# Kernel optimization log

Hardware: AMD Instinct MI355X
Metric: run time of the kernel (lower is better)

## Reference

```python
import jax, jax.numpy as jnp
import numpy as np

B, T, E, H = 4, 2048, 1024, 16
HD = E // H  # head dim = 64

def setup_inputs() -> dict:
    key = jax.random.key(0)
    ks = jax.random.split(key, 5)
    s = 1.0 / np.sqrt(E)
    return {
        "x": jax.random.normal(ks[0], (B, T, E), dtype=jnp.float32),
        "W_attn": jax.random.uniform(ks[1], (E, 3 * E), dtype=jnp.float32, minval=-s, maxval=s),
        "b_attn": jax.random.uniform(ks[2], (3 * E,), dtype=jnp.float32, minval=-s, maxval=s),
        "W_proj": jax.random.uniform(ks[3], (E, E), dtype=jnp.float32, minval=-s, maxval=s),
        "b_proj": jax.random.uniform(ks[4], (E,), dtype=jnp.float32, minval=-s, maxval=s),
    }

def reference(x, W_attn, b_attn, W_proj, b_proj):
    b, t, e = x.shape
    qkv = x @ W_attn + b_attn                      # [B,T,3E]
    q, k, v = jnp.split(qkv, 3, axis=-1)
    # [B,T,E] -> [B,H,T,HD]
    q = q.reshape(b, t, H, HD).transpose(0, 2, 1, 3)
    k = k.reshape(b, t, H, HD).transpose(0, 2, 1, 3)
    v = v.reshape(b, t, H, HD).transpose(0, 2, 1, 3)
    att = jnp.einsum('bhqd,bhkd->bhqk', q, k) * (1.0 / np.sqrt(HD))
    causal_mask = jnp.tril(jnp.ones((t, t), dtype=bool))
    att = jnp.where(causal_mask[None, None, :, :], att, -jnp.inf)
    att = jax.nn.softmax(att, axis=-1)             # drop=0 -> dropout is identity
    y = jnp.einsum('bhqk,bhkd->bhqd', att, v)      # [B,H,T,HD]
    y = y.transpose(0, 2, 1, 3).reshape(b, t, e)
    return y @ W_proj + b_proj
```

## Files before the change

### kernel.cpp

```cpp
#include <hip/hip_runtime.h>
#include <hip/hip_bf16.h>
#include <stdint.h>


#define B_  4
#define T_  2048
#define E_  1024
#define H_  16
#define HD_ 64

typedef unsigned short u16;
typedef __bf16 bf16x8 __attribute__((ext_vector_type(8)));
typedef float f32x4 __attribute__((ext_vector_type(4)));
typedef float f32x16 __attribute__((ext_vector_type(16)));

struct alignas(8) us4 { u16 x, y, z, w; };

__device__ __forceinline__ u16 tobf(float f) {
  union { __bf16 h; u16 u; } c;
  c.h = (__bf16)f;
  return c.u;
}

__device__ __forceinline__ void gload_lds16(const void* g, void* l) {
  auto gp = reinterpret_cast<const __attribute__((address_space(1))) uint32_t*>(
      reinterpret_cast<uintptr_t>(g));
  auto lp = reinterpret_cast<__attribute__((address_space(3))) uint32_t*>(
      reinterpret_cast<uintptr_t>(l));
  __builtin_amdgcn_global_load_lds(gp, lp, 16, 0, 0);
}

__device__ __forceinline__ bf16x8 ld_frag(const u16* p) {
  return *reinterpret_cast<const bf16x8*>(p);
}

#define BARRIER() do { __builtin_amdgcn_s_barrier(); asm volatile("" ::: "memory"); } while (0)


__global__ void cvt_bf16_kernel(const float* __restrict__ in, u16* __restrict__ out, int n) {
  int i = (blockIdx.x * blockDim.x + threadIdx.x) * 4;
  if (i >= n) return;
  float4 v = *reinterpret_cast<const float4*>(in + i);
  us4 o = { tobf(v.x), tobf(v.y), tobf(v.z), tobf(v.w) };
  *reinterpret_cast<us4*>(out + i) = o;
}

__global__ void transpose_cvt_kernel(const float* __restrict__ in, u16* __restrict__ out,
                                     int K, int N) {
  __shared__ u16 tile[32][33];
  int n0 = blockIdx.x * 32, k0 = blockIdx.y * 32;
  int tx = threadIdx.x, ty = threadIdx.y;
#pragma unroll
  for (int i = 0; i < 32; i += 8)
    tile[ty + i][tx] = tobf(in[(size_t)(k0 + ty + i) * N + n0 + tx]);
  __syncthreads();
#pragma unroll
  for (int i = 0; i < 32; i += 8)
    out[(size_t)(n0 + ty + i) * K + k0 + tx] = tile[tx][ty + i];
}


template <int MODE>
__launch_bounds__(512, 2)
__global__ void gemm_kernel(const u16* __restrict__ A, const u16* __restrict__ Bt,
                            const float* __restrict__ bias,
                            u16* __restrict__ qws, u16* __restrict__ kws,
                            u16* __restrict__ vtws, float* __restrict__ out) {
  constexpr int K = 1024, NT = 16;
  __shared__ u16 Asm[3 * 8192];
  __shared__ u16 Bsm[3 * 16384];
  const int tid = threadIdx.x;
  const int wid = tid >> 6, lane = tid & 63;
  const int wm = wid >> 2, wn = wid & 3;
  const int row0 = blockIdx.x * 128, col0 = blockIdx.y * 256;

  const int sgrow = wid * 8 + (lane >> 3);
  const int sgslot = (lane & 7) ^ (lane >> 3);
  const int lrow = lane & 15, lks = lane >> 4, r7 = lrow & 7;
  const int ca0 = ((lks) ^ r7) * 8;
  const int ca1 = ((4 + lks) ^ r7) * 8;
  const int bhalf = (wn >> 1) * 8192 + (wn & 1) * 4096;

#define STG_A(sb, kt, j)                                                        \
  gload_lds16(A + (size_t)(row0 + (j) * 64 + sgrow) * K + (kt) * 64 + sgslot * 8, \
              &Asm[(sb) * 8192 + (j) * 4096 + wid * 512])
#define STG_B(sb, kt, h, j)                                                     \
  gload_lds16(Bt + (size_t)(col0 + (h) * 128 + (j) * 64 + sgrow) * K + (kt) * 64 + sgslot * 8, \
              &Bsm[(sb) * 16384 + (h) * 8192 + (j) * 4096 + wid * 512])
#define RDA(mi, cc) ld_frag(&Asm[rb * 8192 + (wm * 64 + (mi) * 16 + lrow) * 64 + (cc)])
#define RDB(ni, cc) ld_frag(&Bsm[rb * 16384 + bhalf + ((ni) * 16 + lrow) * 64 + (cc)])

  f32x4 acc[4][4] = {};

  STG_A(0, 0, 0); STG_A(0, 0, 1);
  STG_B(0, 0, 0, 0); STG_B(0, 0, 0, 1); STG_B(0, 0, 1, 0); STG_B(0, 0, 1, 1);
  STG_A(1, 1, 0); STG_A(1, 1, 1);
  STG_B(1, 1, 0, 0); STG_B(1, 1, 0, 1); STG_B(1, 1, 1, 0); STG_B(1, 1, 1, 1);
  asm volatile("s_waitcnt vmcnt(6)" ::: "memory");
  BARRIER();

  for (int t = 0; t < NT; ++t) {
    const int rb = t % 3;
    const int sb = (t + 2) % 3;
    const bool hs = (t + 2) < NT;
    const int kt = t + 2;
    bf16x8 af[4], bf[4];

    af[0] = RDA(0, ca0); af[1] = RDA(1, ca0); af[2] = RDA(2, ca0); af[3] = RDA(3, ca0);
    bf[0] = RDB(0, ca0); bf[1] = RDB(1, ca0); bf[2] = RDB(2, ca0); bf[3] = RDB(3, ca0);
    if (hs) { STG_A(sb, kt, 0); STG_A(sb, kt, 1); }
    __builtin_amdgcn_s_setprio(1);
#pragma unroll
    for (int mi = 0; mi < 4; ++mi)
#pragma unroll
      for (int ni = 0; ni < 4; ++ni)
        acc[mi][ni] = __builtin_amdgcn_mfma_f32_16x16x32_bf16(af[mi], bf[ni], acc[mi][ni], 0, 0, 0);
    __builtin_amdgcn_s_setprio(0);

    af[0] = RDA(0, ca1); af[1] = RDA(1, ca1); af[2] = RDA(2, ca1); af[3] = RDA(3, ca1);
    bf[0] = RDB(0, ca1); bf[1] = RDB(1, ca1); bf[2] = RDB(2, ca1); bf[3] = RDB(3, ca1);
    if (hs) { STG_B(sb, kt, 0, 0); STG_B(sb, kt, 0, 1); STG_B(sb, kt, 1, 0); STG_B(sb, kt, 1, 1); }
    __builtin_amdgcn_s_setprio(1);
#pragma unroll
    for (int mi = 0; mi < 4; ++mi)
#pragma unroll
      for (int ni = 0; ni < 4; ++ni)
        acc[mi][ni] = __builtin_amdgcn_mfma_f32_16x16x32_bf16(af[mi], bf[ni], acc[mi][ni], 0, 0, 0);
    __builtin_amdgcn_s_setprio(0);

    if (hs) asm volatile("s_waitcnt vmcnt(6)" ::: "memory");
    else    asm volatile("s_waitcnt vmcnt(0)" ::: "memory");
    BARRIER();
  }
#undef STG_A
#undef STG_B
#undef RDA
#undef RDB

  if constexpr (MODE == 0) {
    const int part = (col0 + wn * 64) >> 10;
    if (part < 2) {
#pragma unroll
      for (int mi = 0; mi < 4; ++mi) {
#pragma unroll
        for (int ni = 0; ni < 4; ++ni) {
          const int gr0 = row0 + wm * 64 + mi * 16 + (lane >> 4) * 4;
          const int gc = col0 + wn * 64 + ni * 16 + (lane & 15);
          const float bv = bias[gc];
          const int e = gc & 1023;
          const int h = e >> 6, d = e & 63;
#pragma unroll
          for (int r = 0; r < 4; ++r) {
            const int m = gr0 + r;
            const int b = m >> 11, tt = m & 2047;
            const float val = acc[mi][ni][r] + bv;
            const size_t bh = (size_t)(b * H_ + h);
            if (part == 0)
              qws[(bh * T_ + tt) * HD_ + d] = tobf(val * 0.1803368801f);
            else
              kws[(bh * T_ + tt) * HD_ + d] = tobf(val);
          }
        }
      }
    } else {
      u16* vt_l = &Bsm[wid * 4608];
#pragma unroll
      for (int mi = 0; mi < 4; ++mi)
#pragma unroll
        for (int ni = 0; ni < 4; ++ni) {
          const float bv = bias[col0 + wn * 64 + ni * 16 + (lane & 15)];
#pragma unroll
          for (int r = 0; r < 4; ++r)
            vt_l[(ni * 16 + (lane & 15)) * 72 + mi * 16 + (lane >> 4) * 4 + r] =
                tobf(acc[mi][ni][r] + bv);
        }
      const int e0 = col0 + wn * 64 - 2048;
      const int h = e0 >> 6;
      const int m0 = row0 + wm * 64;
      const int b = m0 >> 11, tbase = m0 & 2047;
      u16* vbase = vtws + (size_t)(b * H_ + h) * HD_ * T_;
#pragma unroll
      for (int it = 0; it < 8; ++it) {
        const int d = it * 8 + (lane >> 3);
        const uint4 vv = *reinterpret_cast<const uint4*>(&vt_l[d * 72 + (lane & 7) * 8]);
        *reinterpret_cast<uint4*>(&vbase[(size_t)d * T_ + tbase + (lane & 7) * 8]) = vv;
      }
    }
  } else {
#pragma unroll
    for (int mi = 0; mi < 4; ++mi) {
#pragma unroll
      for (int ni = 0; ni < 4; ++ni) {
        const int gr0 = row0 + wm * 64 + mi * 16 + (lane >> 4) * 4;
        const int gc = col0 + wn * 64 + ni * 16 + (lane & 15);
        const float bv = bias[gc];
#pragma unroll
        for (int r = 0; r < 4; ++r)
          out[(size_t)(gr0 + r) * E_ + gc] = acc[mi][ni][r] + bv;
      }
    }
  }
}


__launch_bounds__(256, 4)
__global__ void attn_kernel(const u16* __restrict__ q, const u16* __restrict__ k,
                            const u16* __restrict__ vt, u16* __restrict__ y) {
  __shared__ u16 kl[2][32 * 68];
  __shared__ u16 vl[2][64 * 36];
  const int tid = threadIdx.x, w = tid >> 6, lane = tid & 63;
  const int l31 = lane & 31, hi = lane >> 5;
  const bool H = hi != 0;
  const int bid = blockIdx.x;
  const int j = 15 - (bid >> 6);
  const int bh = bid & 63;
  const u16* qp = q + (size_t)bh * T_ * HD_;
  const u16* kp = k + (size_t)bh * T_ * HD_;
  const u16* vp = vt + (size_t)bh * HD_ * T_;
  const int b = bh >> 4, h = bh & 15;
  u16* yb = y + (size_t)b * T_ * E_ + h * HD_;

  const int t0 = j * 128;
  const int qbw = t0 + w * 32;
  const int nblk = (t0 + 128) >> 5;

  bf16x8 aq[4];
#pragma unroll
  for (int slot = 0; slot < 4; ++slot)
    aq[slot] = ld_frag(qp + (size_t)(qbw + l31) * HD_ + slot * 16 + hi * 8);

  f32x16 o0 = {}, o1 = {};
  float mr = -1e30f, lr = 0.f;

  const int skv = w * 8 + (lane >> 3);
  const int skc = (lane & 7) * 8;
  const int svd = w * 16 + (lane >> 2);
  const int svc = (lane & 3) * 8;

  uint4 kreg = *(const uint4*)(kp + (size_t)skv * HD_ + skc);
  uint4 vreg = *(const uint4*)(vp + (size_t)svd * T_ + svc);

  int buf = 0;
  for (int kb = 0; kb < nblk; ++kb) {
    const int kv0 = kb * 32;
    {
      u16* kd = &kl[buf][skv * 68 + skc];
      uint2 ka = {kreg.x, kreg.y}, kb2 = {kreg.z, kreg.w};
      *(uint2*)kd = ka;
      *(uint2*)(kd + 4) = kb2;
      u16* vd = &vl[buf][svd * 36 + svc];
      uint2 va = {vreg.x, vreg.y}, vb2 = {vreg.z, vreg.w};
      *(uint2*)vd = va;
      *(uint2*)(vd + 4) = vb2;
    }
    if (kb + 1 < nblk) {
      const int kvn = kv0 + 32;
      kreg = *(const uint4*)(kp + (size_t)(kvn + skv) * HD_ + skc);
      vreg = *(const uint4*)(vp + (size_t)svd * T_ + kvn + svc);
    }
    __syncthreads();

    if (kv0 <= qbw + 31) {
      f32x16 s = {};
      __builtin_amdgcn_s_setprio(1);
#pragma unroll
      for (int slot = 0; slot < 4; ++slot) {
        union { uint2 d[2]; bf16x8 v; } kf;
        const u16* kr = &kl[buf][l31 * 68 + slot * 16 + hi * 8];
        kf.d[0] = *(const uint2*)kr;
        kf.d[1] = *(const uint2*)(kr + 4);
        s = __builtin_amdgcn_mfma_f32_32x32x16_bf16(kf.v, aq[slot], s, 0, 0, 0);
      }
      __builtin_amdgcn_s_setprio(0);

      if (kv0 + 31 > qbw) {
        const int qq = qbw + l31;
#pragma unroll
        for (int r = 0; r < 16; ++r) {
          const int kv = kv0 + (r & 3) + 8 * (r >> 2) + 4 * hi;
          if (kv > qq) s[r] = -1e30f;
        }
      }

      float t[8];
#pragma unroll
      for (int r = 0; r < 8; ++r) t[r] = fmaxf(s[r], s[r + 8]);
#pragma unroll
      for (int r = 0; r < 4; ++r) t[r] = fmaxf(t[r], t[r + 4]);
      float pm = fmaxf(fmaxf(t[0], t[1]), fmaxf(t[2], t[3]));
      pm = fmaxf(pm, __shfl_xor(pm, 32));

      if (__any(pm > mr + 8.f)) {
        const float mn = fmaxf(mr, pm);
        const float al = exp2f(mr - mn);
        mr = mn;
        lr *= al;
#pragma unroll
        for (int r = 0; r < 16; ++r) {
          const float ab = __shfl(al, ((r & 3) + 8 * (r >> 2) + 4 * hi) + (lane & 32));
          o0[r] *= ab;
          o1[r] *= ab;
        }
      }

      float p[16];
      float rs = 0.f;
#pragma unroll
      for (int r = 0; r < 16; ++r) {
        p[r] = exp2f(s[r] - mr);
        rs += p[r];
      }
      rs += __shfl_xor(rs, 32);
      lr += rs;

      unsigned cw[8];
#pragma unroll
      for (int i = 0; i < 8; ++i) {
        union { __bf16 hh[2]; unsigned u; } pk;
        pk.hh[0] = (__bf16)p[2 * i];
        pk.hh[1] = (__bf16)p[2 * i + 1];
        cw[i] = pk.u;
      }
      const unsigned r0 = __shfl_xor(H ? cw[0] : cw[2], 32);
      const unsigned r1 = __shfl_xor(H ? cw[1] : cw[3], 32);
      const unsigned r2 = __shfl_xor(H ? cw[4] : cw[6], 32);
      const unsigned r3 = __shfl_xor(H ? cw[5] : cw[7], 32);
      union PU { unsigned u[4]; bf16x8 v; } pa0, pa1;
      pa0.u[0] = H ? r0 : cw[0];
      pa0.u[1] = H ? r1 : cw[1];
      pa0.u[2] = H ? cw[2] : r0;
      pa0.u[3] = H ? cw[3] : r1;
      pa1.u[0] = H ? r2 : cw[4];
      pa1.u[1] = H ? r3 : cw[5];
      pa1.u[2] = H ? cw[6] : r2;
      pa1.u[3] = H ? cw[7] : r3;

      __builtin_amdgcn_s_setprio(1);
      {
        union { uint2 d[2]; bf16x8 v; } vf;
        const u16* vr0 = &vl[buf][l31 * 36 + hi * 8];
        vf.d[0] = *(const uint2*)vr0;
        vf.d[1] = *(const uint2*)(vr0 + 4);
        o0 = __builtin_amdgcn_mfma_f32_32x32x16_bf16(pa0.v, vf.v, o0, 0, 0, 0);
        vf.d[0] = *(const uint2*)(vr0 + 16);
        vf.d[1] = *(const uint2*)(vr0 + 20);
        o0 = __builtin_amdgcn_mfma_f32_32x32x16_bf16(pa1.v, vf.v, o0, 0, 0, 0);
        const u16* vr1 = &vl[buf][(32 + l31) * 36 + hi * 8];
        vf.d[0] = *(const uint2*)vr1;
        vf.d[1] = *(const uint2*)(vr1 + 4);
        o1 = __builtin_amdgcn_mfma_f32_32x32x16_bf16(pa0.v, vf.v, o1, 0, 0, 0);
        vf.d[0] = *(const uint2*)(vr1 + 16);
        vf.d[1] = *(const uint2*)(vr1 + 20);
        o1 = __builtin_amdgcn_mfma_f32_32x32x16_bf16(pa1.v, vf.v, o1, 0, 0, 0);
      }
      __builtin_amdgcn_s_setprio(0);
    }
    buf ^= 1;
  }

  const float il = 1.f / lr;
#pragma unroll
  for (int r = 0; r < 16; ++r) {
    const int cr = (r & 3) + 8 * (r >> 2) + 4 * hi;
    const float li = __shfl(il, cr + (lane & 32));
    const size_t row = (size_t)(qbw + cr) * E_;
    yb[row + l31] = tobf(o0[r] * li);
    yb[row + 32 + l31] = tobf(o1[r] * li);
  }
}


extern "C" void kernel_launch(void* const* d_in, const int* in_sizes, int n_in,
                              void* d_out, int out_size, void* d_ws, size_t ws_size,
                              hipStream_t stream) {
  const float* x  = (const float*)d_in[0];
  const float* Wa = (const float*)d_in[1];
  const float* ba = (const float*)d_in[2];
  const float* Wp = (const float*)d_in[3];
  const float* bp = (const float*)d_in[4];
  float* out = (float*)d_out;

  u16* ws   = (u16*)d_ws;
  u16* xb   = ws;
  u16* waT  = xb  + (size_t)8 * 1024 * 1024;
  u16* wpT  = waT + (size_t)3 * 1024 * 1024;
  u16* qws  = wpT + (size_t)1024 * 1024;
  u16* kws  = qws + (size_t)8 * 1024 * 1024;
  u16* vtws = kws + (size_t)8 * 1024 * 1024;
  u16* yws  = xb;

  cvt_bf16_kernel<<<dim3(8192), dim3(256), 0, stream>>>(x, xb, 8 * 1024 * 1024);
  transpose_cvt_kernel<<<dim3(96, 32), dim3(32, 8), 0, stream>>>(Wa, waT, 1024, 3072);
  transpose_cvt_kernel<<<dim3(32, 32), dim3(32, 8), 0, stream>>>(Wp, wpT, 1024, 1024);

  gemm_kernel<0><<<dim3(64, 12), dim3(512), 0, stream>>>(xb, waT, ba, qws, kws, vtws, nullptr);
  attn_kernel<<<dim3(1024), dim3(256), 0, stream>>>(qws, kws, vtws, yws);
  gemm_kernel<1><<<dim3(64, 4), dim3(512), 0, stream>>>(yws, wpT, bp, nullptr, nullptr, nullptr, out);
}
```

Measured before the change: 182.3 us.

## Stage 64-key KV tiles per barrier and reorder causal block scheduling

The attention loop now loads a 64-key K/V tile per double-buffered stage and processes it as two 32-key halves, which halves the number of __syncthreads barriers and global-to-LDS staging rounds. Each thread keeps two register prefetch slots for K and V. The block-to-query-tile mapping also changes from a pure longest-first order to a serpentine order (15..12, 8..11, 7..4, 0..3) that interleaves heavy and light causal tiles across waves. In exchange, shared memory per block grows and register pressure rises, which could lower occupancy below the four blocks per CU requested by the launch bounds.

Result: faster. 177.5 us (-2.6%).

```diff
diff --git a/kernel.cpp b/kernel.cpp
--- a/kernel.cpp
+++ b/kernel.cpp
@@ -206,13 +206,14 @@
 __launch_bounds__(256, 4)
 __global__ void attn_kernel(const u16* __restrict__ q, const u16* __restrict__ k,
                             const u16* __restrict__ vt, u16* __restrict__ y) {
-  __shared__ u16 kl[2][32 * 68];
-  __shared__ u16 vl[2][64 * 36];
+  __shared__ u16 kl[2][64 * 68];
+  __shared__ u16 vl[2][64 * 68];
   const int tid = threadIdx.x, w = tid >> 6, lane = tid & 63;
   const int l31 = lane & 31, hi = lane >> 5;
   const bool H = hi != 0;
   const int bid = blockIdx.x;
-  const int j = 15 - (bid >> 6);
+  const int s4 = bid >> 8, a = (bid >> 6) & 3;
+  const int j = (s4 == 0) ? (15 - a) : (s4 == 1) ? (8 + a) : (s4 == 2) ? (7 - a) : a;
   const int bh = bid & 63;
   const u16* qp = q + (size_t)bh * T_ * HD_;
   const u16* kp = k + (size_t)bh * T_ * HD_;
@@ -222,7 +223,7 @@
 
   const int t0 = j * 128;
   const int qbw = t0 + w * 32;
-  const int nblk = (t0 + 128) >> 5;
+  const int npass = (t0 + 128) >> 6;
 
   bf16x8 aq[4];
 #pragma unroll
@@ -232,52 +233,64 @@
   f32x16 o0 = {}, o1 = {};
   float mr = -1e30f, lr = 0.f;
 
-  const int skv = w * 8 + (lane >> 3);
-  const int skc = (lane & 7) * 8;
-  const int svd = w * 16 + (lane >> 2);
-  const int svc = (lane & 3) * 8;
-
-  uint4 kreg = *(const uint4*)(kp + (size_t)skv * HD_ + skc);
-  uint4 vreg = *(const uint4*)(vp + (size_t)svd * T_ + svc);
+  const int srow = w * 8 + (lane >> 3);
+  const int scol = (lane & 7) * 8;
+
+  uint4 kreg[2], vreg[2];
+#pragma unroll
+  for (int c = 0; c < 2; ++c) {
+    kreg[c] = *(const uint4*)(kp + (size_t)(c * 32 + srow) * HD_ + scol);
+    vreg[c] = *(const uint4*)(vp + (size_t)(c * 32 + srow) * T_ + scol);
+  }
 
   int buf = 0;
-  for (int kb = 0; kb < nblk; ++kb) {
-    const int kv0 = kb * 32;
-    {
-      u16* kd = &kl[buf][skv * 68 + skc];
-      uint2 ka = {kreg.x, kreg.y}, kb2 = {kreg.z, kreg.w};
-      *(uint2*)kd = ka;
-      *(uint2*)(kd + 4) = kb2;
-      u16* vd = &vl[buf][svd * 36 + svc];
-      uint2 va = {vreg.x, vreg.y}, vb2 = {vreg.z, vreg.w};
-      *(uint2*)vd = va;
-      *(uint2*)(vd + 4) = vb2;
+  for (int pass = 0; pass < npass; ++pass) {
+    const int kv0 = pass * 64;
+#pragma unroll
+    for (int c = 0; c < 2; ++c) {
+      const int row = c * 32 + srow;
+      u16* kd = &kl[buf][row * 68 + scol];
+      uint2 k0 = {kreg[c].x, kreg[c].y}, k1 = {kreg[c].z, kreg[c].w};
+      *(uint2*)kd = k0;
+      *(uint2*)(kd + 4) = k1;
+      u16* vd = &vl[buf][row * 68 + scol];
+      uint2 v0 = {vreg[c].x, vreg[c].y}, v1 = {vreg[c].z, vreg[c].w};
+      *(uint2*)vd = v0;
+      *(uint2*)(vd + 4) = v1;
     }
-    if (kb + 1 < nblk) {
-      const int kvn = kv0 + 32;
-      kreg = *(const uint4*)(kp + (size_t)(kvn + skv) * HD_ + skc);
-      vreg = *(const uint4*)(vp + (size_t)svd * T_ + kvn + svc);
+    if (pass + 1 < npass) {
+      const int kvn = kv0 + 64;
+#pragma unroll
+      for (int c = 0; c < 2; ++c) {
+        kreg[c] = *(const uint4*)(kp + (size_t)(kvn + c * 32 + srow) * HD_ + scol);
+        vreg[c] = *(const uint4*)(vp + (size_t)(c * 32 + srow) * T_ + kvn + scol);
+      }
     }
     __syncthreads();
 
-    if (kv0 <= qbw + 31) {
+#pragma unroll
+    for (int half = 0; half < 2; ++half) {
+      const int kvh = kv0 + half * 32;
+      if (kvh > qbw + 31) break;
+      const int base = half * 32;
+
       f32x16 s = {};
       __builtin_amdgcn_s_setprio(1);
 #pragma unroll
       for (int slot = 0; slot < 4; ++slot) {
         union { uint2 d[2]; bf16x8 v; } kf;
-        const u16* kr = &kl[buf][l31 * 68 + slot * 16 + hi * 8];
+        const u16* kr = &kl[buf][(base + l31) * 68 + slot * 16 + hi * 8];
         kf.d[0] = *(const uint2*)kr;
         kf.d[1] = *(const uint2*)(kr + 4);
         s = __builtin_amdgcn_mfma_f32_32x32x16_bf16(kf.v, aq[slot], s, 0, 0, 0);
       }
       __builtin_amdgcn_s_setprio(0);
 
-      if (kv0 + 31 > qbw) {
+      if (kvh + 31 > qbw) {
         const int qq = qbw + l31;
 #pragma unroll
         for (int r = 0; r < 16; ++r) {
-          const int kv = kv0 + (r & 3) + 8 * (r >> 2) + 4 * hi;
+          const int kv = kvh + (r & 3) + 8 * (r >> 2) + 4 * hi;
           if (kv > qq) s[r] = -1e30f;
         }
       }
@@ -303,12 +316,11 @@
         }
       }
 
-      float p[16];
       float rs = 0.f;
 #pragma unroll
       for (int r = 0; r < 16; ++r) {
-        p[r] = exp2f(s[r] - mr);
-        rs += p[r];
+        s[r] = exp2f(s[r] - mr);
+        rs += s[r];
       }
       rs += __shfl_xor(rs, 32);
       lr += rs;
@@ -317,8 +329,8 @@
 #pragma unroll
       for (int i = 0; i < 8; ++i) {
         union { __bf16 hh[2]; unsigned u; } pk;
-        pk.hh[0] = (__bf16)p[2 * i];
-        pk.hh[1] = (__bf16)p[2 * i + 1];
+        pk.hh[0] = (__bf16)s[2 * i];
+        pk.hh[1] = (__bf16)s[2 * i + 1];
         cw[i] = pk.u;
       }
       const unsigned r0 = __shfl_xor(H ? cw[0] : cw[2], 32);
@@ -338,14 +350,14 @@
       __builtin_amdgcn_s_setprio(1);
       {
         union { uint2 d[2]; bf16x8 v; } vf;
-        const u16* vr0 = &vl[buf][l31 * 36 + hi * 8];
+        const u16* vr0 = &vl[buf][l31 * 68 + base + hi * 8];
         vf.d[0] = *(const uint2*)vr0;
         vf.d[1] = *(const uint2*)(vr0 + 4);
         o0 = __builtin_amdgcn_mfma_f32_32x32x16_bf16(pa0.v, vf.v, o0, 0, 0, 0);
         vf.d[0] = *(const uint2*)(vr0 + 16);
         vf.d[1] = *(const uint2*)(vr0 + 20);
         o0 = __builtin_amdgcn_mfma_f32_32x32x16_bf16(pa1.v, vf.v, o0, 0, 0, 0);
-        const u16* vr1 = &vl[buf][(32 + l31) * 36 + hi * 8];
+        const u16* vr1 = &vl[buf][(32 + l31) * 68 + base + hi * 8];
         vf.d[0] = *(const uint2*)vr1;
         vf.d[1] = *(const uint2*)(vr1 + 4);
         o1 = __builtin_amdgcn_mfma_f32_32x32x16_bf16(pa0.v, vf.v, o1, 0, 0, 0);
```
